# Kernel tuning notes

Measured on AMD Instinct MI355X. Metric: run time of the kernel, lower is better.

The kernel has to match this reference:

```python
import jax, jax.numpy as jnp
import numpy as np

B, N = 16, 65536
N_BOUND = 50           # n_boundaries, linear spacing in [0, 1]
EMBD_LEN = N_BOUND + 1 # 51 learned bucket vectors
EMBD_DIM = 50
OUT_DIM = 50
HID = 2 * EMBD_DIM + 1 # 101, MLP width


def _xavier(key, shape):
    fan_in, fan_out = shape[1], shape[0]
    std = (2.0 / (fan_in + fan_out)) ** 0.5
    return jax.random.normal(key, shape, jnp.float32) * std


def setup_inputs() -> dict:
    key = jax.random.key(0)
    ks = jax.random.split(key, 6)
    x = jax.random.normal(ks[0], (B, N, 1), jnp.float32)
    boundaries = jnp.linspace(0.0, 1.0, N_BOUND).astype(jnp.float32)
    embd = _xavier(ks[1], (EMBD_LEN, EMBD_DIM))
    embd_oob = _xavier(ks[2], (2, OUT_DIM))
    w1 = _xavier(ks[3], (HID, HID))
    b1 = jnp.zeros((HID,), jnp.float32)
    w2 = _xavier(ks[4], (OUT_DIM, HID))
    b2 = jnp.zeros((OUT_DIM,), jnp.float32)
    return {"x": x, "boundaries": boundaries, "embd": embd,
            "embd_oob": embd_oob, "w1": w1, "b1": b1, "w2": w2, "b2": b2}


def reference(x, boundaries, embd, embd_oob, w1, b1, w2, b2):
    xv = x[..., 0]                                   # (B, N)
    # torch.searchsorted default (right=False) == jnp side='left'
    idx = jnp.searchsorted(boundaries, xv)           # in [0, N_BOUND]
    padded = jnp.concatenate([boundaries[:1], boundaries, boundaries[-1:]])  # (N_BOUND+2,)
    lo = padded[idx]
    hi = padded[idx + 1]
    rng = hi - lo
    # rng==0 only where idx is out-of-range (0 or EMBD_LEN-1); those outputs
    # are overwritten below, so guard the division to stay NaN-free.
    dist = (xv - lo) / jnp.where(rng == 0, 1.0, rng)  # (B, N)
    # in-range bucket indices live in [1, EMBD_LEN-2]; clip so idx+1 gather is safe
    ic = jnp.clip(idx, 1, EMBD_LEN - 2)
    feat = jnp.concatenate([embd[ic], embd[ic + 1], dist[..., None]], axis=-1)  # (B, N, 2*EMBD_DIM+1)
    h = jax.nn.gelu(feat @ w1.T + b1, approximate=False)  # torch nn.GELU = exact erf
    mlp_out = h @ w2.T + b2                           # (B, N, OUT_DIM)
    below = (idx == 0)[..., None]
    above = (idx == EMBD_LEN - 1)[..., None]
    out = jnp.where(below, embd_oob[0], jnp.where(above, embd_oob[1], mlp_out))
    return out
```

## Files before the change

kernel.cpp:

```cpp
#include <hip/hip_runtime.h>
#include <math.h>

#define NB        50
#define ED        50
#define OD        50
#define HID       101
#define K         129
#define NBUCKET   49
#define NSAMP     (NBUCKET * K)
#define NROWS     (NSAMP + 2)
#define ROWSTRIDE 52
#define NP        (16 * 65536)
#define CHUNK     17
#define NCHUNK    8

typedef float    f32x2 __attribute__((ext_vector_type(2)));
typedef _Float16 f16x2 __attribute__((ext_vector_type(2)));

__device__ __align__(16) _Float16 g_table[NROWS * ROWSTRIDE];

__global__ __launch_bounds__(256) void build_table(
    const float* __restrict__ embd,
    const float* __restrict__ embd_oob,
    const float* __restrict__ w1,
    const float* __restrict__ b1,
    const float* __restrict__ w2,
    const float* __restrict__ b2)
{
    const int blk = blockIdx.x;
    const int t   = threadIdx.x;

    if (blk == NBUCKET * NCHUNK) {
        if (t < 2 * OD) {
            const int which = t / OD, o = t - which * OD;
            g_table[(NSAMP + which) * ROWSTRIDE + o] = (_Float16)embd_oob[t];
        }
        return;
    }

    const int bu = blk >> 3;
    const int ch = blk & 7;

    __shared__ union U {
        float w1s[HID * HID];
        struct { float w2s[OD * 104]; float hs[CHUNK * 104]; } p;
    } u;
    __shared__ float zc[224];

    for (int i = t; i < HID * HID; i += 256) u.w1s[i] = w1[i];
    __syncthreads();

    if (t < HID) {
        const float* __restrict__ r  = u.w1s + t * HID;
        const float* __restrict__ ea = embd + (bu + 1) * ED;
        float acc = b1[t];
        #pragma unroll 10
        for (int kk = 0; kk < ED; kk++)
            acc = fmaf(ea[kk], r[kk], fmaf(ea[ED + kk], r[ED + kk], acc));
        zc[t]       = acc;
        zc[112 + t] = r[2 * ED];
    }
    __syncthreads();

    for (int i = t; i < OD * HID; i += 256) {
        const int o = i / HID, j = i - o * HID;
        u.p.w2s[o * 104 + j] = w2[i];
    }

    #pragma unroll
    for (int si = 0; si < CHUNK; si++) {
        const int k = ch * CHUNK + si;
        if (t < HID && k < K) {
            const float dist = (float)k * (1.0f / 128.0f);
            const float z = fmaf(dist, zc[112 + t], zc[t]);
            u.p.hs[si * 104 + t] = 0.5f * z * (1.0f + erff(z * 0.70710678118654752f));
        }
    }
    __syncthreads();

    for (int d = t; d < CHUNK * OD; d += 256) {
        const int si = d / OD, o = d - si * OD;
        const int k = ch * CHUNK + si;
        if (k >= K) continue;
        float acc = b2[o];
        const float4* __restrict__ h4 = (const float4*)(u.p.hs  + si * 104);
        const float4* __restrict__ w4 = (const float4*)(u.p.w2s + o  * 104);
        #pragma unroll
        for (int jj = 0; jj < 25; jj++) {
            const float4 hh = h4[jj], ww = w4[jj];
            acc = fmaf(hh.x, ww.x, acc);
            acc = fmaf(hh.y, ww.y, acc);
            acc = fmaf(hh.z, ww.z, acc);
            acc = fmaf(hh.w, ww.w, acc);
        }
        acc = fmaf(u.p.hs[si * 104 + 100], u.p.w2s[o * 104 + 100], acc);
        g_table[(bu * K + k) * ROWSTRIDE + o] = (_Float16)acc;
    }
}

__global__ __launch_bounds__(256) void embed_main(
    const float* __restrict__ x,
    const float* __restrict__ boundaries,
    float* __restrict__ out)
{
    __shared__ float sB[NB];
    __shared__ int4  s_pk[256];
    const int t = threadIdx.x;
    if (t < NB) sB[t] = boundaries[t];
    __syncthreads();

    const int p = blockIdx.x * 256 + t;
    const float xv = x[p];

    int   row, row1;
    float frac = 0.0f;
    if (xv <= sB[0]) {
        row = NSAMP;     row1 = NSAMP;
    } else if (xv > sB[NB - 1]) {
        row = NSAMP + 1; row1 = NSAMP + 1;
    } else {
        int j = (int)(xv * 49.0f);
        if (j > 48) j = 48;
        const int idx = (xv > sB[j]) ? ((xv > sB[j + 1]) ? j + 2 : j + 1) : j;
        const float lo = sB[idx - 1];
        const float hi = sB[idx];
        const float dist = (xv - lo) / (hi - lo);
        const float tt = dist * 128.0f;
        int k0 = (int)tt;
        if (k0 > 127) k0 = 127;
        frac = tt - (float)k0;
        row  = (idx - 1) * K + k0;
        row1 = row + 1;
    }
    s_pk[t] = make_int4(row * 26, row1 * 26, __float_as_int(frac), 0);
    __syncthreads();

    const f16x2* __restrict__ tabh = (const f16x2*)g_table;
    f32x2* __restrict__ o2 = (f32x2*)out + (size_t)blockIdx.x * 6400;

    #pragma unroll
    for (int i = 0; i < 25; i++) {
        const int e  = i * 256 + t;
        const int pt = e / 25;
        const int c2 = e - pt * 25;
        const int4 pk = s_pk[pt];
        const float fr = __int_as_float(pk.z);
        const f16x2 a = tabh[pk.x + c2];
        const f16x2 b = tabh[pk.y + c2];
        const float ax = (float)a.x, ay = (float)a.y;
        f32x2 r;
        r.x = fmaf(fr, (float)b.x - ax, ax);
        r.y = fmaf(fr, (float)b.y - ay, ay);
        o2[e] = r;
    }
}

extern "C" void kernel_launch(void* const* d_in, const int* in_sizes, int n_in,
                              void* d_out, int out_size, void* d_ws, size_t ws_size,
                              hipStream_t stream) {
    const float* x    = (const float*)d_in[0];
    const float* bnd  = (const float*)d_in[1];
    const float* embd = (const float*)d_in[2];
    const float* oob  = (const float*)d_in[3];
    const float* w1   = (const float*)d_in[4];
    const float* b1   = (const float*)d_in[5];
    const float* w2   = (const float*)d_in[6];
    const float* b2   = (const float*)d_in[7];
    float* out = (float*)d_out;

    build_table<<<NBUCKET * NCHUNK + 1, 256, 0, stream>>>(embd, oob, w1, b1, w2, b2);
    embed_main<<<NP / 256, 256, 0, stream>>>(x, bnd, out);
}
```

Measured before the change: 237.9 us.

## Store interleaved adjacent-sample pairs in table and use nontemporal output stores

The lookup table is rebuilt so that each entry holds the fp16 values for sample k and sample k+1 side by side (f16x4). The main kernel then needs one 8-byte gather per output pair instead of two 4-byte gathers from different rows. Output writes are made nontemporal to reduce cache pollution from the large streaming output. The cost is a table roughly twice as large, plus an extra shared-memory staging pass and a sync in the build kernel.

```diff
diff --git a/kernel.cpp b/kernel.cpp
--- a/kernel.cpp
+++ b/kernel.cpp
@@ -5,19 +5,19 @@
 #define ED        50
 #define OD        50
 #define HID       101
-#define K         129
+#define KPAIR     128
 #define NBUCKET   49
-#define NSAMP     (NBUCKET * K)
-#define NROWS     (NSAMP + 2)
-#define ROWSTRIDE 52
+#define NPAIR     (NBUCKET * KPAIR)
+#define NROWS     (NPAIR + 2)
 #define NP        (16 * 65536)
 #define CHUNK     17
 #define NCHUNK    8
 
 typedef float    f32x2 __attribute__((ext_vector_type(2)));
 typedef _Float16 f16x2 __attribute__((ext_vector_type(2)));
+typedef _Float16 f16x4 __attribute__((ext_vector_type(4)));
 
-__device__ __align__(16) _Float16 g_table[NROWS * ROWSTRIDE];
+__device__ __align__(16) f16x4 g_pair[NROWS * 25];
 
 __global__ __launch_bounds__(256) void build_table(
     const float* __restrict__ embd,
@@ -31,9 +31,14 @@
     const int t   = threadIdx.x;
 
     if (blk == NBUCKET * NCHUNK) {
-        if (t < 2 * OD) {
-            const int which = t / OD, o = t - which * OD;
-            g_table[(NSAMP + which) * ROWSTRIDE + o] = (_Float16)embd_oob[t];
+        if (t < 2 * 25) {
+            const int which = t / 25, c = t - which * 25;
+            const float a0 = embd_oob[which * OD + 2 * c];
+            const float a1 = embd_oob[which * OD + 2 * c + 1];
+            f16x4 vv;
+            vv.x = (_Float16)a0; vv.y = (_Float16)a1;
+            vv.z = (_Float16)a0; vv.w = (_Float16)a1;
+            g_pair[(NPAIR + which) * 25 + c] = vv;
         }
         return;
     }
@@ -43,7 +48,11 @@
 
     __shared__ union U {
         float w1s[HID * HID];
-        struct { float w2s[OD * 104]; float hs[CHUNK * 104]; } p;
+        struct {
+            float    w2s[OD * 104];
+            float    hs[18 * 104];
+            _Float16 hbuf[18 * 52];
+        } p;
     } u;
     __shared__ float zc[224];
 
@@ -68,9 +77,9 @@
     }
 
     #pragma unroll
-    for (int si = 0; si < CHUNK; si++) {
+    for (int si = 0; si < 18; si++) {
         const int k = ch * CHUNK + si;
-        if (t < HID && k < K) {
+        if (t < HID && k <= 128) {
             const float dist = (float)k * (1.0f / 128.0f);
             const float z = fmaf(dist, zc[112 + t], zc[t]);
             u.p.hs[si * 104 + t] = 0.5f * z * (1.0f + erff(z * 0.70710678118654752f));
@@ -78,10 +87,8 @@
     }
     __syncthreads();
 
-    for (int d = t; d < CHUNK * OD; d += 256) {
-        const int si = d / OD, o = d - si * OD;
-        const int k = ch * CHUNK + si;
-        if (k >= K) continue;
+    for (int dd = t; dd < 18 * OD; dd += 256) {
+        const int o = dd / 18, si = dd - o * 18;
         float acc = b2[o];
         const float4* __restrict__ h4 = (const float4*)(u.p.hs  + si * 104);
         const float4* __restrict__ w4 = (const float4*)(u.p.w2s + o  * 104);
@@ -94,7 +101,21 @@
             acc = fmaf(hh.w, ww.w, acc);
         }
         acc = fmaf(u.p.hs[si * 104 + 100], u.p.w2s[o * 104 + 100], acc);
-        g_table[(bu * K + k) * ROWSTRIDE + o] = (_Float16)acc;
+        u.p.hbuf[si * 52 + o] = (_Float16)acc;
+    }
+    __syncthreads();
+
+    const f16x2* __restrict__ hb2 = (const f16x2*)u.p.hbuf;
+    for (int d = t; d < CHUNK * 25; d += 256) {
+        const int si = d / 25, c = d - si * 25;
+        const int k = ch * CHUNK + si;
+        if (k <= 127) {
+            const f16x2 a = hb2[si * 26 + c];
+            const f16x2 b = hb2[(si + 1) * 26 + c];
+            f16x4 vv;
+            vv.x = a.x; vv.y = a.y; vv.z = b.x; vv.w = b.y;
+            g_pair[((bu * KPAIR + k) * 25) + c] = vv;
+        }
     }
 }
 
@@ -104,7 +125,7 @@
     float* __restrict__ out)
 {
     __shared__ float sB[NB];
-    __shared__ int4  s_pk[256];
+    __shared__ int2  s_pk[256];
     const int t = threadIdx.x;
     if (t < NB) sB[t] = boundaries[t];
     __syncthreads();
@@ -112,12 +133,12 @@
     const int p = blockIdx.x * 256 + t;
     const float xv = x[p];
 
-    int   row, row1;
+    int   row;
     float frac = 0.0f;
     if (xv <= sB[0]) {
-        row = NSAMP;     row1 = NSAMP;
+        row = NPAIR;
     } else if (xv > sB[NB - 1]) {
-        row = NSAMP + 1; row1 = NSAMP + 1;
+        row = NPAIR + 1;
     } else {
         int j = (int)(xv * 49.0f);
         if (j > 48) j = 48;
@@ -129,13 +150,12 @@
         int k0 = (int)tt;
         if (k0 > 127) k0 = 127;
         frac = tt - (float)k0;
-        row  = (idx - 1) * K + k0;
-        row1 = row + 1;
+        row  = (idx - 1) * KPAIR + k0;
     }
-    s_pk[t] = make_int4(row * 26, row1 * 26, __float_as_int(frac), 0);
+    s_pk[t] = make_int2(row * 25, __float_as_int(frac));
     __syncthreads();
 
-    const f16x2* __restrict__ tabh = (const f16x2*)g_table;
+    const f16x4* __restrict__ tabp = g_pair;
     f32x2* __restrict__ o2 = (f32x2*)out + (size_t)blockIdx.x * 6400;
 
     #pragma unroll
@@ -143,15 +163,14 @@
         const int e  = i * 256 + t;
         const int pt = e / 25;
         const int c2 = e - pt * 25;
-        const int4 pk = s_pk[pt];
-        const float fr = __int_as_float(pk.z);
-        const f16x2 a = tabh[pk.x + c2];
-        const f16x2 b = tabh[pk.y + c2];
-        const float ax = (float)a.x, ay = (float)a.y;
+        const int2 pk = s_pk[pt];
+        const float fr = __int_as_float(pk.y);
+        const f16x4 v = tabp[pk.x + c2];
+        const float ax = (float)v.x, ay = (float)v.y;
         f32x2 r;
-        r.x = fmaf(fr, (float)b.x - ax, ax);
-        r.y = fmaf(fr, (float)b.y - ay, ay);
-        o2[e] = r;
+        r.x = fmaf(fr, (float)v.z - ax, ax);
+        r.y = fmaf(fr, (float)v.w - ay, ay);
+        __builtin_nontemporal_store(r, &o2[e]);
     }
 }
 
```

Measured after the change: 244.4 us. +2.7%, slower.
